# Kernel optimization log

Measured on AMD Instinct MI355X. Metric: run time of the kernel, lower is better.

Reference implementation:

```python
import jax, jax.numpy as jnp
import numpy as np

NUM_CLASSES = 128  # fixed stand-in for len(torch.unique(targets))
B, N_SUP, N_QRY, D = 16, 4096, 4096, 512


def setup_inputs() -> dict:
    key = jax.random.key(0)
    k1, k2, k3, k4 = jax.random.split(key, 4)
    return {
        "support_embeddings": jax.random.normal(k1, (B, N_SUP, D), dtype=jnp.float32),
        "query_embeddings": jax.random.normal(k2, (B, N_QRY, D), dtype=jnp.float32),
        "support_targets": jax.random.randint(k3, (B, N_SUP), 0, NUM_CLASSES),
        "query_targets": jax.random.randint(k4, (B, N_QRY), 0, NUM_CLASSES),
    }


def _prototypes(emb, tgt):
    # emb: (N, D), tgt: (N,) -> (C, D) class means (scatter-add + count clamp)
    sums = jax.ops.segment_sum(emb, tgt, num_segments=NUM_CLASSES)
    cnt = jax.ops.segment_sum(jnp.ones(tgt.shape, emb.dtype), tgt, num_segments=NUM_CLASSES)
    return sums / jnp.maximum(cnt, 1.0)[:, None]


def reference(support_embeddings, query_embeddings, support_targets, query_targets):
    protos = jax.vmap(_prototypes)(support_embeddings, support_targets)  # (B, C, D)
    # squared euclidean distances (B, C, Nq) via ||p||^2 + ||q||^2 - 2 p.q (GEMM form)
    p_sq = jnp.sum(protos * protos, axis=-1)                      # (B, C)
    q_sq = jnp.sum(query_embeddings * query_embeddings, axis=-1)  # (B, Nq)
    cross = jnp.einsum('bcd,bqd->bcq', protos, query_embeddings)  # (B, C, Nq)
    dist = p_sq[:, :, None] + q_sq[:, None, :] - 2.0 * cross
    predictions = jnp.argmin(dist, axis=1)                        # (B, Nq)
    # F.cross_entropy(-dist, targets): class dim is axis 1
    logp = jax.nn.log_softmax(-dist, axis=1)                      # (B, C, Nq)
    nll = -jnp.take_along_axis(logp, query_targets[:, None, :], axis=1)[:, 0, :]
    loss = jnp.mean(nll)
    accuracy = jnp.mean((predictions == query_targets).astype(jnp.float32))
    return predictions, loss, accuracy
```

## Files before the change

### kernel.cpp

```cpp
#include <hip/hip_runtime.h>
#include <math.h>

#define B_ 16
#define NSUP_ 4096
#define NQ_ 4096
#define D_ 512
#define C_ 128
#define MARGIN 0.02f

typedef __attribute__((ext_vector_type(8))) short bf16x8;
typedef __attribute__((ext_vector_type(4))) float f32x4;

__device__ inline short f2bf(float f) {
    unsigned u = __float_as_uint(f);
    unsigned r = (u + 0x7fffu + ((u >> 16) & 1u)) >> 16;
    return (short)r;
}
__device__ inline float bf2f(short h) {
    return __uint_as_float(((unsigned)(unsigned short)h) << 16);
}
__device__ inline void gload16(const void* g, void* l) {
    __builtin_amdgcn_global_load_lds(
        (const __attribute__((address_space(1))) void*)g,
        (__attribute__((address_space(3))) void*)l, 16, 0, 0);
}
__device__ inline void conv8(const float4& fa, const float4& fb, bf16x8& h8, bf16x8& l8) {
    float xv[8] = {fa.x, fa.y, fa.z, fa.w, fb.x, fb.y, fb.z, fb.w};
    #pragma unroll
    for (int e = 0; e < 8; e++) {
        short hb = f2bf(xv[e]);
        h8[e] = hb;
        l8[e] = f2bf(xv[e] - bf2f(hb));
    }
}

__global__ __launch_bounds__(256) void sort_kernel(
    const int* __restrict__ tgt, int* __restrict__ perm,
    int* __restrict__ class_base, int* __restrict__ class_cnt,
    int* __restrict__ flag_count, int* __restrict__ acc_delta)
{
    __shared__ int cnt[C_];
    __shared__ int base[C_];
    int b = blockIdx.x, tid = threadIdx.x;
    if (tid < C_) cnt[tid] = 0;
    __syncthreads();
    for (int i = tid; i < NSUP_; i += 256) atomicAdd(&cnt[tgt[b * NSUP_ + i]], 1);
    __syncthreads();
    if (tid == 0) { int s = 0; for (int c = 0; c < C_; c++) { base[c] = s; s += cnt[c]; } }
    __syncthreads();
    if (tid < C_) {
        class_base[b * C_ + tid] = base[tid];
        class_cnt [b * C_ + tid] = cnt[tid];
    }
    if (b == 0 && tid == 0) { *flag_count = 0; *acc_delta = 0; }
    __syncthreads();
    for (int i = tid; i < NSUP_; i += 256) {
        int c = tgt[b * NSUP_ + i];
        int pos = atomicAdd(&base[c], 1);
        perm[b * NSUP_ + pos] = i;
    }
}

__global__ __launch_bounds__(256) void proto_kernel(
    const float* __restrict__ sup, const int* __restrict__ class_base,
    const int* __restrict__ class_cnt, const int* __restrict__ perm,
    short* __restrict__ Ahg, short* __restrict__ Alg,
    double* __restrict__ p64, double* __restrict__ psq64, float* __restrict__ psq32)
{
    __shared__ int rows[256];
    __shared__ double sums[2][512];
    __shared__ float pm[512];
    __shared__ double red[128];
    int g = blockIdx.x, b = g >> 7, c = g & 127;
    int tid = threadIdx.x;
    int half = tid >> 7, d0 = (tid & 127) * 4;
    int base = class_base[b * C_ + c], cnt = class_cnt[b * C_ + c];
    const float* eb = sup + (size_t)b * NSUP_ * D_;
    double a0 = 0.0, a1 = 0.0, a2 = 0.0, a3 = 0.0;
    for (int r0 = 0; r0 < cnt; r0 += 256) {
        int nr = min(256, cnt - r0);
        __syncthreads();
        if (tid < nr) rows[tid] = perm[b * NSUP_ + base + r0 + tid];
        __syncthreads();
        for (int r = half; r < nr; r += 2) {
            float4 v = *(const float4*)(eb + (size_t)rows[r] * D_ + d0);
            a0 += (double)v.x; a1 += (double)v.y; a2 += (double)v.z; a3 += (double)v.w;
        }
    }
    sums[half][d0 + 0] = a0; sums[half][d0 + 1] = a1;
    sums[half][d0 + 2] = a2; sums[half][d0 + 3] = a3;
    __syncthreads();
    double cw = (double)(cnt > 1 ? cnt : 1);
    if (tid < 128) {
        double ps = 0.0;
        size_t ob = (size_t)(b * C_ + c) * D_ + d0;
        #pragma unroll
        for (int j = 0; j < 4; j++) {
            double m = (sums[0][d0 + j] + sums[1][d0 + j]) / cw;
            p64[ob + j] = m;
            pm[d0 + j] = (float)m;
            ps += m * m;
        }
        red[tid] = ps;
    }
    __syncthreads();
    for (int s = 64; s > 0; s >>= 1) {
        if (tid < s) red[tid] += red[tid + s];
        __syncthreads();
    }
    if (tid == 0) { psq64[g] = red[0]; psq32[g] = (float)red[0]; }
    if (tid < 64) {
        int ch = tid >> 2, ktile = tid & 3;
        int mt = c >> 4;
        bf16x8 h8, l8;
        #pragma unroll
        for (int e = 0; e < 8; e++) {
            float x = pm[tid * 8 + e];
            short hb = f2bf(x);
            h8[e] = hb;
            l8[e] = f2bf(x - bf2f(hb));
        }
        size_t goff = ((((size_t)b * 16 + ch) * 8 + mt) * 64 + ktile * 16 + (c & 15));
        *(bf16x8*)(Ahg + goff * 8) = h8;
        *(bf16x8*)(Alg + goff * 8) = l8;
    }
}

__global__ __launch_bounds__(256) void screen_kernel(
    const float* __restrict__ qry, const int* __restrict__ qtgt,
    const short* __restrict__ Ahg, const short* __restrict__ Alg,
    const float* __restrict__ psq32,
    float* __restrict__ out_pred, double* __restrict__ blk_loss,
    float* __restrict__ blk_acc, int* __restrict__ flags, int* __restrict__ flag_count)
{
    __shared__ __align__(16) short Ah[2][4096];
    __shared__ __align__(16) short Al[2][4096];
    __shared__ __align__(16) short Bh[2][4096];
    __shared__ __align__(16) short Bl[2][4096];
    __shared__ float ldsPsq[C_];
    __shared__ double wl[4];
    __shared__ float  wa[4];

    int blk = blockIdx.x;
    int b   = blk >> 5;
    int qb  = (blk & 31) * 128;
    int tid = threadIdx.x;
    int wave = tid >> 6, lane = tid & 63;
    int quad = lane >> 4, n16 = lane & 15;

    if (tid < C_) ldsPsq[tid] = psq32[b * C_ + tid];

    f32x4 acc[8][2];
    #pragma unroll
    for (int mt = 0; mt < 8; mt++)
        #pragma unroll
        for (int nt = 0; nt < 2; nt++)
            acc[mt][nt] = (f32x4){0.f, 0.f, 0.f, 0.f};

    const float* qbB = qry + ((size_t)b * NQ_ + qb) * D_;
    const short* AhB = Ahg + (size_t)b * 16 * 4096;
    const short* AlB = Alg + (size_t)b * 16 * 4096;

    const int G0 = tid, G1 = tid + 256;
    const float* bsrc0 = qbB + (size_t)(((G0 >> 6) << 4) + (G0 & 15)) * D_ + (((G0 >> 4) & 3) << 3);
    const float* bsrc1 = qbB + (size_t)(((G1 >> 6) << 4) + (G1 & 15)) * D_ + (((G1 >> 4) & 3) << 3);

    float4 bq0a, bq0b, bq1a, bq1b;

    bq0a = *(const float4*)(bsrc0);
    bq0b = *(const float4*)(bsrc0 + 4);
    bq1a = *(const float4*)(bsrc1);
    bq1b = *(const float4*)(bsrc1 + 4);
    {
        char* dh = (char*)&Ah[0][0];
        char* dl = (char*)&Al[0][0];
        gload16(AhB + tid * 8,        dh + tid * 16);
        gload16(AhB + 2048 + tid * 8, dh + 4096 + tid * 16);
        gload16(AlB + tid * 8,        dl + tid * 16);
        gload16(AlB + 2048 + tid * 8, dl + 4096 + tid * 16);
    }
    {
        bf16x8 h8, l8;
        conv8(bq0a, bq0b, h8, l8);
        *(bf16x8*)&Bh[0][G0 * 8] = h8;
        *(bf16x8*)&Bl[0][G0 * 8] = l8;
    }
    {
        bf16x8 h8, l8;
        conv8(bq1a, bq1b, h8, l8);
        *(bf16x8*)&Bh[0][G1 * 8] = h8;
        *(bf16x8*)&Bl[0][G1 * 8] = l8;
    }
    __syncthreads();

    #pragma unroll 2
    for (int ch = 0; ch < 16; ch++) {
        int p = ch & 1;
        if (ch < 15) {
            int cn = ch + 1;
            bq0a = *(const float4*)(bsrc0 + cn * 32);
            bq0b = *(const float4*)(bsrc0 + cn * 32 + 4);
            bq1a = *(const float4*)(bsrc1 + cn * 32);
            bq1b = *(const float4*)(bsrc1 + cn * 32 + 4);
            const short* sh = AhB + cn * 4096;
            const short* sl = AlB + cn * 4096;
            char* dh = (char*)&Ah[p ^ 1][0];
            char* dl = (char*)&Al[p ^ 1][0];
            gload16(sh + tid * 8,        dh + tid * 16);
            gload16(sh + 2048 + tid * 8, dh + 4096 + tid * 16);
            gload16(sl + tid * 8,        dl + tid * 16);
            gload16(sl + 2048 + tid * 8, dl + 4096 + tid * 16);
        }
        int nt0 = wave * 2, nt1 = nt0 + 1;
        bf16x8 bh0 = *(const bf16x8*)&Bh[p][(nt0 * 64 + lane) * 8];
        bf16x8 bl0 = *(const bf16x8*)&Bl[p][(nt0 * 64 + lane) * 8];
        bf16x8 bh1 = *(const bf16x8*)&Bh[p][(nt1 * 64 + lane) * 8];
        bf16x8 bl1 = *(const bf16x8*)&Bl[p][(nt1 * 64 + lane) * 8];
        #pragma unroll
        for (int mt = 0; mt < 8; mt++) {
            bf16x8 ah = *(const bf16x8*)&Ah[p][(mt * 64 + lane) * 8];
            bf16x8 al = *(const bf16x8*)&Al[p][(mt * 64 + lane) * 8];
            acc[mt][0] = __builtin_amdgcn_mfma_f32_16x16x32_bf16(ah, bh0, acc[mt][0], 0, 0, 0);
            acc[mt][0] = __builtin_amdgcn_mfma_f32_16x16x32_bf16(ah, bl0, acc[mt][0], 0, 0, 0);
            acc[mt][0] = __builtin_amdgcn_mfma_f32_16x16x32_bf16(al, bh0, acc[mt][0], 0, 0, 0);
            acc[mt][1] = __builtin_amdgcn_mfma_f32_16x16x32_bf16(ah, bh1, acc[mt][1], 0, 0, 0);
            acc[mt][1] = __builtin_amdgcn_mfma_f32_16x16x32_bf16(ah, bl1, acc[mt][1], 0, 0, 0);
            acc[mt][1] = __builtin_amdgcn_mfma_f32_16x16x32_bf16(al, bh1, acc[mt][1], 0, 0, 0);
        }
        if (ch < 15) {
            {
                bf16x8 h8, l8;
                conv8(bq0a, bq0b, h8, l8);
                *(bf16x8*)&Bh[p ^ 1][G0 * 8] = h8;
                *(bf16x8*)&Bl[p ^ 1][G0 * 8] = l8;
            }
            {
                bf16x8 h8, l8;
                conv8(bq1a, bq1b, h8, l8);
                *(bf16x8*)&Bh[p ^ 1][G1 * 8] = h8;
                *(bf16x8*)&Bl[p ^ 1][G1 * 8] = l8;
            }
        }
        __syncthreads();
    }

    float4 psqv[8];
    #pragma unroll
    for (int mt = 0; mt < 8; mt++)
        psqv[mt] = *(const float4*)&ldsPsq[mt * 16 + quad * 4];

    double wloss = 0.0; float wacc = 0.0f;

    #pragma unroll
    for (int nt = 0; nt < 2; nt++) {
        int ntg = wave * 2 + nt;
        int qloc = ntg * 16 + n16;
        int gq = b * NQ_ + qb + qloc;
        int tq = qtgt[gq];

        float b1 = 1e30f, b2 = 1e30f, dt = 1e30f, lm = -1e30f;
        int c1 = 0;
        #pragma unroll
        for (int mt = 0; mt < 8; mt++) {
            #pragma unroll
            for (int r = 0; r < 4; r++) {
                float d = psqv[mt][r] - 2.0f * acc[mt][nt][r];
                int c = mt * 16 + quad * 4 + r;
                if (d < b1) { b2 = b1; b1 = d; c1 = c; }
                else if (d < b2) { b2 = d; }
                lm = fmaxf(lm, -d);
                if (c == tq) dt = d;
            }
        }
        float ls = 0.0f;
        #pragma unroll
        for (int mt = 0; mt < 8; mt++) {
            #pragma unroll
            for (int r = 0; r < 4; r++) {
                float d = psqv[mt][r] - 2.0f * acc[mt][nt][r];
                ls += __expf(-d - lm);
            }
        }
        #pragma unroll
        for (int off = 16; off <= 32; off <<= 1) {
            float o1 = __shfl_xor(b1, off, 64);
            int   oc = __shfl_xor(c1, off, 64);
            float o2 = __shfl_xor(b2, off, 64);
            float n2 = fminf(fmaxf(b1, o1), fminf(b2, o2));
            if (o1 < b1 || (o1 == b1 && oc < c1)) { b1 = o1; c1 = oc; }
            b2 = n2;
            float om = __shfl_xor(lm, off, 64);
            float os = __shfl_xor(ls, off, 64);
            float nm = fmaxf(lm, om);
            ls = ls * __expf(lm - nm) + os * __expf(om - nm);
            lm = nm;
            dt = fminf(dt, __shfl_xor(dt, off, 64));
        }
        if (quad == 0) {
            wloss += (double)(dt + lm) + (double)logf(ls);
            wacc  += (c1 == tq) ? 1.0f : 0.0f;
            out_pred[gq] = (float)c1;
            if (b2 - b1 < MARGIN) {
                int pos = atomicAdd(flag_count, 1);
                flags[pos] = gq;
            }
        }
    }

    #pragma unroll
    for (int off = 1; off <= 8; off <<= 1) {
        wloss += __shfl_xor(wloss, off, 64);
        wacc  += __shfl_xor(wacc,  off, 64);
    }
    if (lane == 0) { wl[wave] = wloss; wa[wave] = wacc; }
    __syncthreads();
    if (tid == 0) {
        blk_loss[blk] = wl[0] + wl[1] + wl[2] + wl[3];
        blk_acc[blk]  = wa[0] + wa[1] + wa[2] + wa[3];
    }
}

__global__ __launch_bounds__(256) void rescue_kernel(
    const float* __restrict__ qry, const int* __restrict__ qtgt,
    const double* __restrict__ p64, const double* __restrict__ psq64,
    const int* __restrict__ flags, const int* __restrict__ flag_count,
    float* __restrict__ out_pred, int* __restrict__ acc_delta)
{
    int tid = threadIdx.x, wave = tid >> 6, lane = tid & 63;
    int cnt = *flag_count;
    for (int f = blockIdx.x * 4 + wave; f < cnt; f += 1024) {
        int gq = flags[f];
        int b  = gq >> 12;
        const float* qp = qry + (size_t)gq * D_;
        float4 qa = *(const float4*)(qp + 8 * lane);
        float4 qb4 = *(const float4*)(qp + 8 * lane + 4);
        double q[8] = {(double)qa.x,(double)qa.y,(double)qa.z,(double)qa.w,
                       (double)qb4.x,(double)qb4.y,(double)qb4.z,(double)qb4.w};
        double qsq = 0.0;
        #pragma unroll
        for (int k = 0; k < 8; k++) qsq = fma(q[k], q[k], qsq);
        for (int off = 32; off; off >>= 1) qsq += __shfl_xor(qsq, off, 64);

        const double* pb = p64 + (size_t)b * C_ * D_;
        double bd = 1e300; int bc = 0;
        for (int c = 0; c < C_; c += 2) {
            const double* pr0 = pb + (size_t)c * D_ + 8 * lane;
            const double* pr1 = pr0 + D_;
            double dot0 = 0.0, dot1 = 0.0;
            #pragma unroll
            for (int k = 0; k < 8; k++) {
                dot0 = fma(pr0[k], q[k], dot0);
                dot1 = fma(pr1[k], q[k], dot1);
            }
            for (int off = 32; off; off >>= 1) {
                dot0 += __shfl_xor(dot0, off, 64);
                dot1 += __shfl_xor(dot1, off, 64);
            }
            double d0 = psq64[b * C_ + c]     + qsq - 2.0 * dot0;
            double d1 = psq64[b * C_ + c + 1] + qsq - 2.0 * dot1;
            if (d0 < bd) { bd = d0; bc = c; }
            if (d1 < bd) { bd = d1; bc = c + 1; }
        }
        if (lane == 0) {
            int tq = qtgt[gq];
            int oldc = (int)out_pred[gq];
            if (oldc != bc) {
                out_pred[gq] = (float)bc;
                int delta = ((bc == tq) ? 1 : 0) - ((oldc == tq) ? 1 : 0);
                if (delta) atomicAdd(acc_delta, delta);
            }
        }
    }
}

__global__ __launch_bounds__(256) void finalize_kernel(
    const double* __restrict__ blk_loss, const float* __restrict__ blk_acc,
    const int* __restrict__ acc_delta, float* __restrict__ out)
{
    __shared__ double rl[256];
    __shared__ float  ra[256];
    int tid = threadIdx.x;
    double s = 0.0; float a = 0.0f;
    for (int i = tid; i < 512; i += 256) { s += blk_loss[i]; a += blk_acc[i]; }
    rl[tid] = s; ra[tid] = a;
    __syncthreads();
    for (int st = 128; st; st >>= 1) {
        if (tid < st) { rl[tid] += rl[tid + st]; ra[tid] += ra[tid + st]; }
        __syncthreads();
    }
    if (tid == 0) {
        out[B_*NQ_    ] = (float)(rl[0] / (double)(B_ * NQ_));
        out[B_*NQ_ + 1] = (ra[0] + (float)(*acc_delta)) / (float)(B_ * NQ_);
    }
}

extern "C" void kernel_launch(void* const* d_in, const int* in_sizes, int n_in,
                              void* d_out, int out_size, void* d_ws, size_t ws_size,
                              hipStream_t stream) {
    const float* sup  = (const float*)d_in[0];
    const float* qry  = (const float*)d_in[1];
    const int*   stgt = (const int*)d_in[2];
    const int*   qtgt = (const int*)d_in[3];
    float* out = (float*)d_out;

    char* ws = (char*)d_ws;
    constexpr size_t O_P64   = 0;
    constexpr size_t O_AH    = O_P64   + 8388608;
    constexpr size_t O_AL    = O_AH    + 2097152;
    constexpr size_t O_PSQ64 = O_AL    + 2097152;
    constexpr size_t O_PSQ32 = O_PSQ64 + 16384;
    constexpr size_t O_CBASE = O_PSQ32 + 8192;
    constexpr size_t O_CCNT  = O_CBASE + 8192;
    constexpr size_t O_PERM  = O_CCNT  + 8192;
    constexpr size_t O_BLOSS = O_PERM  + 262144;
    constexpr size_t O_BACC  = O_BLOSS + 4096;
    constexpr size_t O_FLAGS = O_BACC  + 2048;
    constexpr size_t O_CNT   = O_FLAGS + 262144;

    double* p64       = (double*)(ws + O_P64);
    short*  Ahg       = (short*) (ws + O_AH);
    short*  Alg       = (short*) (ws + O_AL);
    double* psq64     = (double*)(ws + O_PSQ64);
    float*  psq32     = (float*) (ws + O_PSQ32);
    int*    cbase     = (int*)   (ws + O_CBASE);
    int*    ccnt      = (int*)   (ws + O_CCNT);
    int*    perm      = (int*)   (ws + O_PERM);
    double* blk_loss  = (double*)(ws + O_BLOSS);
    float*  blk_acc   = (float*) (ws + O_BACC);
    int*    flags     = (int*)   (ws + O_FLAGS);
    int*    flag_count= (int*)   (ws + O_CNT);
    int*    acc_delta = flag_count + 1;

    hipLaunchKernelGGL(sort_kernel,   dim3(16),   dim3(256), 0, stream,
                       stgt, perm, cbase, ccnt, flag_count, acc_delta);
    hipLaunchKernelGGL(proto_kernel,  dim3(2048), dim3(256), 0, stream,
                       sup, cbase, ccnt, perm, Ahg, Alg, p64, psq64, psq32);
    hipLaunchKernelGGL(screen_kernel, dim3(512),  dim3(256), 0, stream,
                       qry, qtgt, Ahg, Alg, psq32, out, blk_loss, blk_acc, flags, flag_count);
    hipLaunchKernelGGL(rescue_kernel, dim3(256),  dim3(256), 0, stream,
                       qry, qtgt, p64, psq64, flags, flag_count, out, acc_delta);
    hipLaunchKernelGGL(finalize_kernel, dim3(1),  dim3(256), 0, stream,
                       blk_loss, blk_acc, acc_delta, out);
}
```

Measured before the change: 382.8 us.

## Deepen screen pipeline, vectorize sort, unroll proto gather, fuse finalize into rescue

Reworks the screen GEMM main loop so query loads for the chunk two steps ahead are issued earlier, using two register sets and manual unrolling by two. The goal is to hide global load latency behind the MFMA work. The sort kernel now reads targets as int4 and keeps one histogram per wave to reduce LDS atomic contention. The proto gather now has two independent accumulator chains, and the finalize kernel is merged into rescue through a last-block counter, removing one launch. The extra live registers may lower occupancy, and the last-block pattern depends on correct fencing.

```diff
diff --git a/kernel.cpp b/kernel.cpp
--- a/kernel.cpp
+++ b/kernel.cpp
@@ -37,27 +37,43 @@
 __global__ __launch_bounds__(256) void sort_kernel(
     const int* __restrict__ tgt, int* __restrict__ perm,
     int* __restrict__ class_base, int* __restrict__ class_cnt,
-    int* __restrict__ flag_count, int* __restrict__ acc_delta)
+    int* __restrict__ flag_count, int* __restrict__ acc_delta, int* __restrict__ done_ctr)
 {
-    __shared__ int cnt[C_];
+    __shared__ int cnt4[4][C_];
     __shared__ int base[C_];
     int b = blockIdx.x, tid = threadIdx.x;
-    if (tid < C_) cnt[tid] = 0;
-    __syncthreads();
-    for (int i = tid; i < NSUP_; i += 256) atomicAdd(&cnt[tgt[b * NSUP_ + i]], 1);
-    __syncthreads();
-    if (tid == 0) { int s = 0; for (int c = 0; c < C_; c++) { base[c] = s; s += cnt[c]; } }
-    __syncthreads();
-    if (tid < C_) {
-        class_base[b * C_ + tid] = base[tid];
-        class_cnt [b * C_ + tid] = cnt[tid];
-    }
-    if (b == 0 && tid == 0) { *flag_count = 0; *acc_delta = 0; }
-    __syncthreads();
-    for (int i = tid; i < NSUP_; i += 256) {
-        int c = tgt[b * NSUP_ + i];
-        int pos = atomicAdd(&base[c], 1);
-        perm[b * NSUP_ + pos] = i;
+    int wv = tid >> 6;
+    #pragma unroll
+    for (int i = tid; i < 4 * C_; i += 256) ((int*)cnt4)[i] = 0;
+    __syncthreads();
+    const int4* t4 = (const int4*)(tgt + b * NSUP_);
+    for (int i = tid; i < NSUP_ / 4; i += 256) {
+        int4 v = t4[i];
+        atomicAdd(&cnt4[wv][v.x], 1);
+        atomicAdd(&cnt4[wv][v.y], 1);
+        atomicAdd(&cnt4[wv][v.z], 1);
+        atomicAdd(&cnt4[wv][v.w], 1);
+    }
+    __syncthreads();
+    if (tid == 0) {
+        int s = 0;
+        for (int c = 0; c < C_; c++) {
+            int cc = cnt4[0][c] + cnt4[1][c] + cnt4[2][c] + cnt4[3][c];
+            base[c] = s;
+            class_base[b * C_ + c] = s;
+            class_cnt [b * C_ + c] = cc;
+            s += cc;
+        }
+    }
+    if (b == 0 && tid == 0) { *flag_count = 0; *acc_delta = 0; *done_ctr = 0; }
+    __syncthreads();
+    for (int i = tid; i < NSUP_ / 4; i += 256) {
+        int4 v = t4[i];
+        int i0 = 4 * i;
+        int p0 = atomicAdd(&base[v.x], 1); perm[b * NSUP_ + p0] = i0;
+        int p1 = atomicAdd(&base[v.y], 1); perm[b * NSUP_ + p1] = i0 + 1;
+        int p2 = atomicAdd(&base[v.z], 1); perm[b * NSUP_ + p2] = i0 + 2;
+        int p3 = atomicAdd(&base[v.w], 1); perm[b * NSUP_ + p3] = i0 + 3;
     }
 }
 
@@ -77,18 +93,26 @@
     int base = class_base[b * C_ + c], cnt = class_cnt[b * C_ + c];
     const float* eb = sup + (size_t)b * NSUP_ * D_;
     double a0 = 0.0, a1 = 0.0, a2 = 0.0, a3 = 0.0;
+    double b0 = 0.0, b1 = 0.0, b2 = 0.0, b3 = 0.0;
     for (int r0 = 0; r0 < cnt; r0 += 256) {
         int nr = min(256, cnt - r0);
         __syncthreads();
         if (tid < nr) rows[tid] = perm[b * NSUP_ + base + r0 + tid];
         __syncthreads();
-        for (int r = half; r < nr; r += 2) {
-            float4 v = *(const float4*)(eb + (size_t)rows[r] * D_ + d0);
-            a0 += (double)v.x; a1 += (double)v.y; a2 += (double)v.z; a3 += (double)v.w;
-        }
-    }
-    sums[half][d0 + 0] = a0; sums[half][d0 + 1] = a1;
-    sums[half][d0 + 2] = a2; sums[half][d0 + 3] = a3;
+        int r = half;
+        for (; r + 2 < nr; r += 4) {
+            float4 v0 = *(const float4*)(eb + (size_t)rows[r] * D_ + d0);
+            float4 v1 = *(const float4*)(eb + (size_t)rows[r + 2] * D_ + d0);
+            a0 += (double)v0.x; a1 += (double)v0.y; a2 += (double)v0.z; a3 += (double)v0.w;
+            b0 += (double)v1.x; b1 += (double)v1.y; b2 += (double)v1.z; b3 += (double)v1.w;
+        }
+        if (r < nr) {
+            float4 v0 = *(const float4*)(eb + (size_t)rows[r] * D_ + d0);
+            a0 += (double)v0.x; a1 += (double)v0.y; a2 += (double)v0.z; a3 += (double)v0.w;
+        }
+    }
+    sums[half][d0 + 0] = a0 + b0; sums[half][d0 + 1] = a1 + b1;
+    sums[half][d0 + 2] = a2 + b2; sums[half][d0 + 3] = a3 + b3;
     __syncthreads();
     double cw = (double)(cnt > 1 ? cnt : 1);
     if (tid < 128) {
@@ -165,84 +189,76 @@
     const float* bsrc0 = qbB + (size_t)(((G0 >> 6) << 4) + (G0 & 15)) * D_ + (((G0 >> 4) & 3) << 3);
     const float* bsrc1 = qbB + (size_t)(((G1 >> 6) << 4) + (G1 & 15)) * D_ + (((G1 >> 4) & 3) << 3);
 
-    float4 bq0a, bq0b, bq1a, bq1b;
-
-    bq0a = *(const float4*)(bsrc0);
-    bq0b = *(const float4*)(bsrc0 + 4);
-    bq1a = *(const float4*)(bsrc1);
-    bq1b = *(const float4*)(bsrc1 + 4);
-    {
-        char* dh = (char*)&Ah[0][0];
-        char* dl = (char*)&Al[0][0];
-        gload16(AhB + tid * 8,        dh + tid * 16);
-        gload16(AhB + 2048 + tid * 8, dh + 4096 + tid * 16);
-        gload16(AlB + tid * 8,        dl + tid * 16);
-        gload16(AlB + 2048 + tid * 8, dl + 4096 + tid * 16);
-    }
-    {
-        bf16x8 h8, l8;
-        conv8(bq0a, bq0b, h8, l8);
-        *(bf16x8*)&Bh[0][G0 * 8] = h8;
-        *(bf16x8*)&Bl[0][G0 * 8] = l8;
-    }
-    {
-        bf16x8 h8, l8;
-        conv8(bq1a, bq1b, h8, l8);
-        *(bf16x8*)&Bh[0][G1 * 8] = h8;
-        *(bf16x8*)&Bl[0][G1 * 8] = l8;
-    }
-    __syncthreads();
-
-    #pragma unroll 2
-    for (int ch = 0; ch < 16; ch++) {
-        int p = ch & 1;
-        if (ch < 15) {
-            int cn = ch + 1;
-            bq0a = *(const float4*)(bsrc0 + cn * 32);
-            bq0b = *(const float4*)(bsrc0 + cn * 32 + 4);
-            bq1a = *(const float4*)(bsrc1 + cn * 32);
-            bq1b = *(const float4*)(bsrc1 + cn * 32 + 4);
-            const short* sh = AhB + cn * 4096;
-            const short* sl = AlB + cn * 4096;
-            char* dh = (char*)&Ah[p ^ 1][0];
-            char* dl = (char*)&Al[p ^ 1][0];
-            gload16(sh + tid * 8,        dh + tid * 16);
-            gload16(sh + 2048 + tid * 8, dh + 4096 + tid * 16);
-            gload16(sl + tid * 8,        dl + tid * 16);
-            gload16(sl + 2048 + tid * 8, dl + 4096 + tid * 16);
-        }
-        int nt0 = wave * 2, nt1 = nt0 + 1;
-        bf16x8 bh0 = *(const bf16x8*)&Bh[p][(nt0 * 64 + lane) * 8];
-        bf16x8 bl0 = *(const bf16x8*)&Bl[p][(nt0 * 64 + lane) * 8];
-        bf16x8 bh1 = *(const bf16x8*)&Bh[p][(nt1 * 64 + lane) * 8];
-        bf16x8 bl1 = *(const bf16x8*)&Bl[p][(nt1 * 64 + lane) * 8];
-        #pragma unroll
-        for (int mt = 0; mt < 8; mt++) {
-            bf16x8 ah = *(const bf16x8*)&Ah[p][(mt * 64 + lane) * 8];
-            bf16x8 al = *(const bf16x8*)&Al[p][(mt * 64 + lane) * 8];
-            acc[mt][0] = __builtin_amdgcn_mfma_f32_16x16x32_bf16(ah, bh0, acc[mt][0], 0, 0, 0);
-            acc[mt][0] = __builtin_amdgcn_mfma_f32_16x16x32_bf16(ah, bl0, acc[mt][0], 0, 0, 0);
-            acc[mt][0] = __builtin_amdgcn_mfma_f32_16x16x32_bf16(al, bh0, acc[mt][0], 0, 0, 0);
-            acc[mt][1] = __builtin_amdgcn_mfma_f32_16x16x32_bf16(ah, bh1, acc[mt][1], 0, 0, 0);
-            acc[mt][1] = __builtin_amdgcn_mfma_f32_16x16x32_bf16(ah, bl1, acc[mt][1], 0, 0, 0);
-            acc[mt][1] = __builtin_amdgcn_mfma_f32_16x16x32_bf16(al, bh1, acc[mt][1], 0, 0, 0);
-        }
-        if (ch < 15) {
-            {
-                bf16x8 h8, l8;
-                conv8(bq0a, bq0b, h8, l8);
-                *(bf16x8*)&Bh[p ^ 1][G0 * 8] = h8;
-                *(bf16x8*)&Bl[p ^ 1][G0 * 8] = l8;
-            }
-            {
-                bf16x8 h8, l8;
-                conv8(bq1a, bq1b, h8, l8);
-                *(bf16x8*)&Bh[p ^ 1][G1 * 8] = h8;
-                *(bf16x8*)&Bl[p ^ 1][G1 * 8] = l8;
-            }
-        }
-        __syncthreads();
-    }
+    float4 eA0, eA1, eA2, eA3;
+    float4 eB0, eB1, eB2, eB3;
+
+#define LOADB(SET, CH) { \
+        const float* s0_ = bsrc0 + (CH) * 32; \
+        const float* s1_ = bsrc1 + (CH) * 32; \
+        e##SET##0 = *(const float4*)(s0_); \
+        e##SET##1 = *(const float4*)(s0_ + 4); \
+        e##SET##2 = *(const float4*)(s1_); \
+        e##SET##3 = *(const float4*)(s1_ + 4); }
+
+#define WRITEB(SET, BUF) { \
+        bf16x8 h8_, l8_; \
+        conv8(e##SET##0, e##SET##1, h8_, l8_); \
+        *(bf16x8*)&Bh[BUF][G0 * 8] = h8_; \
+        *(bf16x8*)&Bl[BUF][G0 * 8] = l8_; \
+        conv8(e##SET##2, e##SET##3, h8_, l8_); \
+        *(bf16x8*)&Bh[BUF][G1 * 8] = h8_; \
+        *(bf16x8*)&Bl[BUF][G1 * 8] = l8_; }
+
+#define GLOADA(CH, BUF) { \
+        const short* sh_ = AhB + (CH) * 4096; \
+        const short* sl_ = AlB + (CH) * 4096; \
+        char* dh_ = (char*)&Ah[BUF][0]; \
+        char* dl_ = (char*)&Al[BUF][0]; \
+        gload16(sh_ + tid * 8,        dh_ + tid * 16); \
+        gload16(sh_ + 2048 + tid * 8, dh_ + 4096 + tid * 16); \
+        gload16(sl_ + tid * 8,        dl_ + tid * 16); \
+        gload16(sl_ + 2048 + tid * 8, dl_ + 4096 + tid * 16); }
+
+#define COMPUTE(BUF) { \
+        int nt0_ = wave * 2, nt1_ = nt0_ + 1; \
+        bf16x8 bh0 = *(const bf16x8*)&Bh[BUF][(nt0_ * 64 + lane) * 8]; \
+        bf16x8 bl0 = *(const bf16x8*)&Bl[BUF][(nt0_ * 64 + lane) * 8]; \
+        bf16x8 bh1 = *(const bf16x8*)&Bh[BUF][(nt1_ * 64 + lane) * 8]; \
+        bf16x8 bl1 = *(const bf16x8*)&Bl[BUF][(nt1_ * 64 + lane) * 8]; \
+        _Pragma("unroll") \
+        for (int mt = 0; mt < 8; mt++) { \
+            bf16x8 ah = *(const bf16x8*)&Ah[BUF][(mt * 64 + lane) * 8]; \
+            bf16x8 al = *(const bf16x8*)&Al[BUF][(mt * 64 + lane) * 8]; \
+            acc[mt][0] = __builtin_amdgcn_mfma_f32_16x16x32_bf16(ah, bh0, acc[mt][0], 0, 0, 0); \
+            acc[mt][0] = __builtin_amdgcn_mfma_f32_16x16x32_bf16(ah, bl0, acc[mt][0], 0, 0, 0); \
+            acc[mt][0] = __builtin_amdgcn_mfma_f32_16x16x32_bf16(al, bh0, acc[mt][0], 0, 0, 0); \
+            acc[mt][1] = __builtin_amdgcn_mfma_f32_16x16x32_bf16(ah, bh1, acc[mt][1], 0, 0, 0); \
+            acc[mt][1] = __builtin_amdgcn_mfma_f32_16x16x32_bf16(ah, bl1, acc[mt][1], 0, 0, 0); \
+            acc[mt][1] = __builtin_amdgcn_mfma_f32_16x16x32_bf16(al, bh1, acc[mt][1], 0, 0, 0); \
+        } }
+
+    LOADB(A, 0);
+    GLOADA(0, 0);
+    WRITEB(A, 0);
+    LOADB(B, 1);
+    __syncthreads();
+
+    for (int ch = 0; ch < 16; ch += 2) {
+        if (ch + 2 < 16) LOADB(A, ch + 2);
+        WRITEB(B, 1);
+        if (ch + 1 < 16) GLOADA(ch + 1, 1);
+        COMPUTE(0);
+        __syncthreads();
+        if (ch + 3 < 16) LOADB(B, ch + 3);
+        if (ch + 2 < 16) { WRITEB(A, 0); GLOADA(ch + 2, 0); }
+        COMPUTE(1);
+        __syncthreads();
+    }
+
+#undef LOADB
+#undef WRITEB
+#undef GLOADA
+#undef COMPUTE
 
     float4 psqv[8];
     #pragma unroll
@@ -320,11 +336,13 @@
     }
 }
 
-__global__ __launch_bounds__(256) void rescue_kernel(
+__global__ __launch_bounds__(256) void rescue_finalize_kernel(
     const float* __restrict__ qry, const int* __restrict__ qtgt,
     const double* __restrict__ p64, const double* __restrict__ psq64,
     const int* __restrict__ flags, const int* __restrict__ flag_count,
-    float* __restrict__ out_pred, int* __restrict__ acc_delta)
+    float* __restrict__ out_pred, int* __restrict__ acc_delta,
+    const double* __restrict__ blk_loss, const float* __restrict__ blk_acc,
+    int* __restrict__ done_ctr, float* __restrict__ out)
 {
     int tid = threadIdx.x, wave = tid >> 6, lane = tid & 63;
     int cnt = *flag_count;
@@ -371,26 +389,28 @@
             }
         }
     }
-}
-
-__global__ __launch_bounds__(256) void finalize_kernel(
-    const double* __restrict__ blk_loss, const float* __restrict__ blk_acc,
-    const int* __restrict__ acc_delta, float* __restrict__ out)
-{
-    __shared__ double rl[256];
-    __shared__ float  ra[256];
-    int tid = threadIdx.x;
-    double s = 0.0; float a = 0.0f;
-    for (int i = tid; i < 512; i += 256) { s += blk_loss[i]; a += blk_acc[i]; }
-    rl[tid] = s; ra[tid] = a;
-    __syncthreads();
-    for (int st = 128; st; st >>= 1) {
-        if (tid < st) { rl[tid] += rl[tid + st]; ra[tid] += ra[tid + st]; }
-        __syncthreads();
-    }
-    if (tid == 0) {
-        out[B_*NQ_    ] = (float)(rl[0] / (double)(B_ * NQ_));
-        out[B_*NQ_ + 1] = (ra[0] + (float)(*acc_delta)) / (float)(B_ * NQ_);
+
+    __shared__ int amlast;
+    __syncthreads();
+    __threadfence();
+    if (tid == 0) amlast = (atomicAdd(done_ctr, 1) == 255) ? 1 : 0;
+    __syncthreads();
+    if (amlast) {
+        __threadfence();
+        __shared__ double rl[256];
+        __shared__ float  ra[256];
+        double s = 0.0; float a = 0.0f;
+        for (int i = tid; i < 512; i += 256) { s += blk_loss[i]; a += blk_acc[i]; }
+        rl[tid] = s; ra[tid] = a;
+        __syncthreads();
+        for (int st = 128; st; st >>= 1) {
+            if (tid < st) { rl[tid] += rl[tid + st]; ra[tid] += ra[tid + st]; }
+            __syncthreads();
+        }
+        if (tid == 0) {
+            out[B_*NQ_    ] = (float)(rl[0] / (double)(B_ * NQ_));
+            out[B_*NQ_ + 1] = (ra[0] + (float)(*acc_delta)) / (float)(B_ * NQ_);
+        }
     }
 }
 
@@ -430,15 +450,15 @@
     int*    flags     = (int*)   (ws + O_FLAGS);
     int*    flag_count= (int*)   (ws + O_CNT);
     int*    acc_delta = flag_count + 1;
+    int*    done_ctr  = flag_count + 2;
 
     hipLaunchKernelGGL(sort_kernel,   dim3(16),   dim3(256), 0, stream,
-                       stgt, perm, cbase, ccnt, flag_count, acc_delta);
+                       stgt, perm, cbase, ccnt, flag_count, acc_delta, done_ctr);
     hipLaunchKernelGGL(proto_kernel,  dim3(2048), dim3(256), 0, stream,
                        sup, cbase, ccnt, perm, Ahg, Alg, p64, psq64, psq32);
     hipLaunchKernelGGL(screen_kernel, dim3(512),  dim3(256), 0, stream,
                        qry, qtgt, Ahg, Alg, psq32, out, blk_loss, blk_acc, flags, flag_count);
-    hipLaunchKernelGGL(rescue_kernel, dim3(256),  dim3(256), 0, stream,
-                       qry, qtgt, p64, psq64, flags, flag_count, out, acc_delta);
-    hipLaunchKernelGGL(finalize_kernel, dim3(1),  dim3(256), 0, stream,
-                       blk_loss, blk_acc, acc_delta, out);
-}
+    hipLaunchKernelGGL(rescue_finalize_kernel, dim3(256), dim3(256), 0, stream,
+                       qry, qtgt, p64, psq64, flags, flag_count, out, acc_delta,
+                       blk_loss, blk_acc, done_ctr, out);
+}
```

Result: slower. 394.3 us (+3.0%).
